# Performance work log

Measured on AMD Instinct MI355X. Metric: run time of the kernel, lower is better.

## Reference

```python
import jax, jax.numpy as jnp
import numpy as np

jax.config.update("jax_enable_x64", True)  # faithful int64 LIF state, as in the torch module

NUM_INPUTS = 700
NUM_HIDDEN = 4096
NUM_OUTPUT = 20
N_STEPS = 1000
ALPHA_SHIFT = 4   # synaptic-current decay shift
BETA_SHIFT = 3    # membrane decay shift
THRESHOLD = 1
BW1 = 64
BW2 = 64


def _sat(x, bw):
    # Quantize.saturate + to_int: clamp to signed bw-bit range, cast to int64.
    lo = -(2 ** (bw - 1))
    hi = 2 ** (bw - 1) - 1
    if jnp.issubdtype(x.dtype, jnp.floating):
        # values here are far below 2**63, so the float clip/cast is exact
        return jnp.clip(x, float(lo), float(hi)).astype(jnp.int64)
    return jnp.clip(x, lo, hi)


def _decay(v, shift):
    # LIF.exp_decay: v - (v >> shift) with arithmetic right shift on int64
    return v - (v >> shift)


def setup_inputs() -> dict:
    key = jax.random.key(0)
    k1, k2, k3, k4 = jax.random.split(key, 4)
    input_spikes = jax.random.randint(k1, (N_STEPS, NUM_INPUTS), 0, 2, dtype=jnp.int64)
    w1 = jax.random.randint(k2, (NUM_HIDDEN, NUM_INPUTS), -8, 8, dtype=jnp.int64)
    v1 = jax.random.randint(k3, (NUM_HIDDEN, NUM_HIDDEN), -8, 8, dtype=jnp.int64)
    w2 = jax.random.randint(k4, (NUM_OUTPUT, NUM_HIDDEN), -8, 8, dtype=jnp.int64)
    return {"input_spikes": input_spikes, "w1": w1, "v1": v1, "w2": w2}


def reference(input_spikes, w1, v1, w2):
    w1f = w1.astype(jnp.float32)
    v1f = v1.astype(jnp.float32)
    w2f = w2.astype(jnp.float32)
    # feed-forward input currents for all timesteps at once: [T, H]
    in_all = _sat(jnp.einsum("hi,ti->th", w1f, input_spikes.astype(jnp.float32)), BW1)

    H = w1.shape[0]
    O = w2.shape[0]
    z = lambda n: jnp.zeros((n,), dtype=jnp.int64)
    # state: hidden spikes, hidden mem, hidden syn, readout mem, readout syn
    init = (z(H), z(H), z(H), z(O), z(O))

    def step(state, in_cur):
        h_out, h_mem, h_syn, r_mem, r_syn = state
        # recurrent feedback current from PREVIOUS step's hidden spikes
        fb = _sat(jnp.einsum("hk,k->h", v1f, h_out.astype(jnp.float32)), BW1)
        syn_curr = _sat(in_cur + fb, BW1)
        # hidden LIF: reset (by previous spike) -> threshold -> decay/integrate
        h_mem = jnp.where(h_out == 1, 0, h_mem)
        new_out = (h_mem - THRESHOLD > 0).astype(jnp.int64)
        new_mem = _decay(h_mem, BETA_SHIFT) + h_syn
        new_syn = _decay(h_syn, ALPHA_SHIFT) + syn_curr
        # readout LIF (no reset); records updated membrane
        ro_cur = _sat(jnp.einsum("oh,h->o", w2f, new_out.astype(jnp.float32)), BW2)
        new_rmem = _decay(r_mem, BETA_SHIFT) + r_syn
        new_rsyn = _decay(r_syn, ALPHA_SHIFT) + ro_cur
        return (new_out, new_mem, new_syn, new_rmem, new_rsyn), new_rmem

    _, rec = jax.lax.scan(step, init, in_all)  # rec: [T, O]
    return rec.T  # torch.stack(ro_mem_rec, dim=1) -> [num_output, n_steps]
```

## Files before the change

### kernel.cpp

```cpp
#include <hip/hip_runtime.h>

#define T_STEPS 1000
#define N_IN    700
#define N_HID   4096
#define N_OUT   20
#define NBLK    64
#define HPB     64

typedef unsigned int u32x4 __attribute__((ext_vector_type(4)));

__device__ __forceinline__ u32x4 load_rec_sync(const u32x4* p) {
    u32x4 r;
    asm volatile("global_load_dwordx4 %0, %1, off sc0 sc1\n\t"
                 "s_waitcnt vmcnt(0)"
                 : "=v"(r) : "v"(p) : "memory");
    return r;
}
__device__ __forceinline__ void store_rec(u32x4* p, u32x4 v) {
    asm volatile("global_store_dwordx4 %0, %1, off sc0 sc1"
                 :: "v"(p), "v"(v) : "memory");
}

__global__ __launch_bounds__(256) void k_transpose_i8(
    const int* __restrict__ in, signed char* __restrict__ out,
    int R, int C, int out_stride)
{
    __shared__ signed char tile[32][33];
    const int cx = blockIdx.x * 32;
    const int ry = blockIdx.y * 32;
    const int tx = threadIdx.x;
    const int ty = threadIdx.y;
#pragma unroll
    for (int r = 0; r < 4; ++r) {
        int row = ry + ty + r * 8;
        int col = cx + tx;
        if (row < R && col < C)
            tile[ty + r * 8][tx] = (signed char)in[(size_t)row * C + col];
    }
    __syncthreads();
#pragma unroll
    for (int r = 0; r < 4; ++r) {
        int c   = cx + ty + r * 8;
        int row = ry + tx;
        if (c < C && row < R)
            out[(size_t)c * out_stride + row] = tile[tx][ty + r * 8];
    }
}

__global__ __launch_bounds__(256) void k_prep_v1(
    const int* __restrict__ in, unsigned char* __restrict__ out)
{
    __shared__ unsigned char tile[32][33];
    const int kx = blockIdx.x * 32;
    const int hy = blockIdx.y * 32;
    const int tx = threadIdx.x;
    const int ty = threadIdx.y;
#pragma unroll
    for (int r = 0; r < 4; ++r) {
        int h = hy + ty + r * 8;
        tile[ty + r * 8][tx] = (unsigned char)(in[(size_t)h * N_HID + kx + tx] + 8);
    }
    __syncthreads();
    const size_t bofs = (size_t)(hy >> 6) * (N_HID * 64) + (hy & 32);
#pragma unroll
    for (int r = 0; r < 4; ++r) {
        int k = kx + ty + r * 8;
        out[bofs + ((size_t)k << 6) + tx] = tile[tx][ty + r * 8];
    }
}

__global__ __launch_bounds__(256) void k_inall(
    const signed char* __restrict__ w1t,
    const int* __restrict__ spk,
    short* __restrict__ in_all2)
{
    __shared__ int s_spk[16][N_IN];
    const int t0 = blockIdx.y * 16;
    const int tcnt = min(16, T_STEPS - t0);
    const int tid = threadIdx.x;
    for (int b = 0; b < tcnt; ++b)
        for (int i = tid; i < N_IN; i += 256)
            s_spk[b][i] = spk[(size_t)(t0 + b) * N_IN + i];
    __syncthreads();
    const int h = blockIdx.x * 256 + tid;
    int acc[16];
#pragma unroll
    for (int b = 0; b < 16; ++b) acc[b] = 0;
    for (int i = 0; i < N_IN; ++i) {
        int w = (int)w1t[(size_t)i * N_HID + h];
#pragma unroll
        for (int b = 0; b < 16; ++b) acc[b] += w * s_spk[b][i];
    }
    const size_t base = (size_t)(h >> 6) * (T_STEPS * 64) + (h & 63);
    for (int b = 0; b < tcnt; ++b)
        in_all2[base + (size_t)(t0 + b) * 64] = (short)acc[b];
}

__global__ __launch_bounds__(256) void k_main(
    const short* __restrict__ in_all2,
    const unsigned char* __restrict__ v1b,
    u32x4* __restrict__ pub)
{
    const int tid  = threadIdx.x;
    const int wave = tid >> 6;
    const int lane = tid & 63;
    const int bid  = blockIdx.x;

    __shared__ u32x4 s_rec[2][NBLK];
    __shared__ unsigned int s_part[2][4][4][8];
    __shared__ int s_nw[2][4];

    int mm = 0, synv = 0, out_t = 0;

    const int mb = (wave << 4) | (lane >> 2);
    const unsigned char* gslot =
        v1b + ((size_t)bid << 18) + ((size_t)mb << 12) + ((lane & 3) << 4);
    const short* in_base = in_all2 + (size_t)bid * (T_STEPS * 64) + lane;

    if (tid == 0) { u32x4 v = {0u, 0u, 1u, 0u}; store_rec(pub + bid, v); }
    __syncthreads();

    for (int t = 0; t < T_STEPS; ++t) {
        const int cur = t & 1;
        int in_cur = 0;
        if (wave == 0) {
            int mem_t = (mm - (mm >> 3)) + synv;
            int mnext = out_t ? 0 : mem_t;
            int out_n = (mnext - 1 > 0) ? 1 : 0;
            unsigned long long om = __ballot(out_n);
            if (lane == 0) {
                u32x4 v = {(unsigned)om, (unsigned)(om >> 32), 1u, 0u};
                store_rec(pub + (size_t)(t + 1) * NBLK + bid, v);
            }
            in_cur = (int)in_base[t * 64];
            mm = mnext; out_t = out_n;
            __builtin_amdgcn_global_load_lds(
                (const void*)(pub + (size_t)t * NBLK + lane),
                (void*)&s_rec[cur ^ 1][0], 16, 0,  17);
        }

        unsigned int mlo = 0, mhi = 0;
        if (t > 0) {
            u32x4 rec = s_rec[cur][mb];
            if (rec.z == 0u) {
                const u32x4* rp = pub + (size_t)(t - 1) * NBLK + mb;
                do { __builtin_amdgcn_s_sleep(1); rec = load_rec_sync(rp); }
                while (rec.z == 0u);
            }
            mlo = rec.x; mhi = rec.y;
        }
        int myc = __popc(mlo) + __popc(mhi);

        unsigned int a0=0,a1=0,a2=0,a3=0,a4=0,a5=0,a6=0,a7=0;
        const unsigned int M = 0x00FF00FFu;
        {
            unsigned int m0 = mlo;
            while (m0) {
                int b = __builtin_ctz(m0); m0 &= m0 - 1;
                u32x4 v = *(const u32x4*)(gslot + ((size_t)b << 6));
                a0 += v.x & M;  a1 += (v.x >> 8) & M;
                a2 += v.y & M;  a3 += (v.y >> 8) & M;
                a4 += v.z & M;  a5 += (v.z >> 8) & M;
                a6 += v.w & M;  a7 += (v.w >> 8) & M;
            }
            unsigned int m1 = mhi;
            while (m1) {
                int b = __builtin_ctz(m1); m1 &= m1 - 1;
                u32x4 v = *(const u32x4*)(gslot + ((size_t)(b + 32) << 6));
                a0 += v.x & M;  a1 += (v.x >> 8) & M;
                a2 += v.y & M;  a3 += (v.y >> 8) & M;
                a4 += v.z & M;  a5 += (v.z >> 8) & M;
                a6 += v.w & M;  a7 += (v.w >> 8) & M;
            }
        }
#pragma unroll
        for (int s = 4; s <= 32; s <<= 1) {
            a0 += __shfl_xor(a0, s); a1 += __shfl_xor(a1, s);
            a2 += __shfl_xor(a2, s); a3 += __shfl_xor(a3, s);
            a4 += __shfl_xor(a4, s); a5 += __shfl_xor(a5, s);
            a6 += __shfl_xor(a6, s); a7 += __shfl_xor(a7, s);
            myc += __shfl_xor(myc, s);
        }
        if (lane == 0) s_nw[cur][wave] = myc;
        if (lane < 4) {
            unsigned int* sp = s_part[cur][wave][lane];
            sp[0]=a0; sp[1]=a1; sp[2]=a2; sp[3]=a3;
            sp[4]=a4; sp[5]=a5; sp[6]=a6; sp[7]=a7;
        }
        __syncthreads();

        if (wave == 0) {
            const int n = s_nw[cur][0] + s_nw[cur][1] + s_nw[cur][2] + s_nw[cur][3];
            const int li = lane >> 4, b = lane & 15;
            const int c = ((b >> 2) << 1) | (b & 1);
            const int half = (b >> 1) & 1;
            unsigned int s = s_part[cur][0][li][c] + s_part[cur][1][li][c]
                           + s_part[cur][2][li][c] + s_part[cur][3][li][c];
            int fb = (int)((s >> (half << 4)) & 0xFFFFu) - 8 * n;
            synv = (synv - (synv >> 4)) + in_cur + fb;
        }
    }
}

__global__ __launch_bounds__(256) void k_rocur(
    const int* __restrict__ w2,
    const u32x4* __restrict__ pub,
    int* __restrict__ ro)
{
    const int t = blockIdx.x;
    const int tid = threadIdx.x;
    __shared__ unsigned short s_list[N_HID];
    __shared__ int s_red[32][8];
    __shared__ int s_n;
    if (tid < 64) {
        u32x4 rec = pub[(size_t)t * NBLK + tid];
        unsigned long long m = (unsigned long long)rec.x |
                               ((unsigned long long)rec.y << 32);
        int cnt = __popcll(m);
        int inc = cnt;
#pragma unroll
        for (int d = 1; d < 64; d <<= 1) {
            int v = __shfl_up(inc, d);
            if (tid >= d) inc += v;
        }
        int p = inc - cnt;
        while (m) {
            s_list[p++] = (unsigned short)((tid << 6) | __builtin_ctzll(m));
            m &= m - 1;
        }
        if (tid == 63) s_n = inc;
    }
    __syncthreads();
    const int n = s_n;
    const int o = tid >> 3;
    const int r = tid & 7;
    if (o < N_OUT) {
        int acc = 0;
        for (int j = r; j < n; j += 8) acc += w2[(size_t)o * N_HID + s_list[j]];
        s_red[o][r] = acc;
    }
    __syncthreads();
    if (tid < N_OUT) {
        int acc = 0;
#pragma unroll
        for (int q = 0; q < 8; ++q) acc += s_red[tid][q];
        ro[(size_t)t * N_OUT + tid] = acc;
    }
}

#define CH 250
__global__ __launch_bounds__(256) void k_scan(const int* __restrict__ ro,
                                              int* __restrict__ out)
{
    __shared__ int s_ro[CH * N_OUT];
    __shared__ int s_out[CH * N_OUT];
    const int tid = threadIdx.x;
    int rm = 0, rs = 0;
    for (int c = 0; c < T_STEPS / CH; ++c) {
        for (int i = tid; i < CH * N_OUT; i += 256)
            s_ro[i] = ro[c * CH * N_OUT + i];
        __syncthreads();
        if (tid < N_OUT) {
            for (int j = 0; j < CH; ++j) {
                rm = (rm - (rm >> 3)) + rs;
                rs = (rs - (rs >> 4)) + s_ro[j * N_OUT + tid];
                s_out[j * N_OUT + tid] = rm;
            }
        }
        __syncthreads();
        for (int i = tid; i < CH * N_OUT; i += 256) {
            int o = i / CH, j = i - o * CH;
            out[o * T_STEPS + c * CH + j] = s_out[j * N_OUT + o];
        }
        __syncthreads();
    }
}

extern "C" void kernel_launch(void* const* d_in, const int* in_sizes, int n_in,
                              void* d_out, int out_size, void* d_ws, size_t ws_size,
                              hipStream_t stream)
{
    const int* spk = (const int*)d_in[0];
    const int* w1  = (const int*)d_in[1];
    const int* v1  = (const int*)d_in[2];
    const int* w2  = (const int*)d_in[3];
    int* out = (int*)d_out;

    char* ws = (char*)d_ws;
    constexpr size_t SZ_PUB    = (size_t)(T_STEPS + 1) * NBLK * 16;
    constexpr size_t OFF_PUB   = 0;
    constexpr size_t OFF_INALL = OFF_PUB + SZ_PUB;
    constexpr size_t OFF_V1B   = OFF_INALL + 8192000;
    constexpr size_t OFF_W1T   = OFF_V1B + 16777216;
    constexpr size_t OFF_RO    = OFF_W1T + 2867200;

    u32x4*          pub    = (u32x4*)(ws + OFF_PUB);
    short*          in_all = (short*)(ws + OFF_INALL);
    unsigned char*  v1b    = (unsigned char*)(ws + OFF_V1B);
    signed char*    w1t    = (signed char*)(ws + OFF_W1T);
    int*            ro     = (int*)(ws + OFF_RO);

    hipMemsetAsync(pub, 0, SZ_PUB, stream);

    dim3 tb(32, 8);
    k_prep_v1<<<dim3(128, 128), tb, 0, stream>>>(v1, v1b);
    k_transpose_i8<<<dim3(22, 128), tb, 0, stream>>>(w1, w1t, N_HID, N_IN, N_HID);
    k_inall<<<dim3(16, 63), 256, 0, stream>>>(w1t, spk, in_all);

    k_main<<<dim3(NBLK), dim3(256), 0, stream>>>(in_all, v1b, pub);

    k_rocur<<<dim3(T_STEPS), 256, 0, stream>>>(w2, pub, ro);
    k_scan<<<1, 256, 0, stream>>>(ro, out);
}
```

Measured before the change: 1.661 ms.

## Split recurrence across 256 single-wave blocks with nibble-packed weights in LDS

```diff
diff --git a/kernel.cpp b/kernel.cpp
--- a/kernel.cpp
+++ b/kernel.cpp
@@ -4,20 +4,21 @@
 #define N_IN    700
 #define N_HID   4096
 #define N_OUT   20
-#define NBLK    64
-#define HPB     64
+#define NBLK    256
+#define NPB     16
 
 typedef unsigned int u32x4 __attribute__((ext_vector_type(4)));
-
-__device__ __forceinline__ u32x4 load_rec_sync(const u32x4* p) {
-    u32x4 r;
-    asm volatile("global_load_dwordx4 %0, %1, off sc0 sc1\n\t"
+typedef unsigned int u32x2 __attribute__((ext_vector_type(2)));
+
+__device__ __forceinline__ unsigned load_rec4(const unsigned* p) {
+    unsigned r;
+    asm volatile("global_load_dword %0, %1, off sc0 sc1\n\t"
                  "s_waitcnt vmcnt(0)"
                  : "=v"(r) : "v"(p) : "memory");
     return r;
 }
-__device__ __forceinline__ void store_rec(u32x4* p, u32x4 v) {
-    asm volatile("global_store_dwordx4 %0, %1, off sc0 sc1"
+__device__ __forceinline__ void store_rec4(unsigned* p, unsigned v) {
+    asm volatile("global_store_dword %0, %1, off sc0 sc1"
                  :: "v"(p), "v"(v) : "memory");
 }
 
@@ -47,25 +48,28 @@
     }
 }
 
-__global__ __launch_bounds__(256) void k_prep_v1(
+__global__ __launch_bounds__(256) void k_prep_v1n(
     const int* __restrict__ in, unsigned char* __restrict__ out)
 {
-    __shared__ unsigned char tile[32][33];
-    const int kx = blockIdx.x * 32;
-    const int hy = blockIdx.y * 32;
-    const int tx = threadIdx.x;
-    const int ty = threadIdx.y;
+    __shared__ unsigned char tile[16][64];
+    const int k0 = blockIdx.x * 64;
+    const int b  = blockIdx.y;
+    const int t  = threadIdx.x;
+    const int kk = t & 63;
 #pragma unroll
     for (int r = 0; r < 4; ++r) {
-        int h = hy + ty + r * 8;
-        tile[ty + r * 8][tx] = (unsigned char)(in[(size_t)h * N_HID + kx + tx] + 8);
-    }
-    __syncthreads();
-    const size_t bofs = (size_t)(hy >> 6) * (N_HID * 64) + (hy & 32);
-#pragma unroll
-    for (int r = 0; r < 4; ++r) {
-        int k = kx + ty + r * 8;
-        out[bofs + ((size_t)k << 6) + tx] = tile[tx][ty + r * 8];
+        int hl = (t >> 6) + r * 4;
+        tile[hl][kk] = (unsigned char)(in[(size_t)(b * NPB + hl) * N_HID + k0 + kk] + 8);
+    }
+    __syncthreads();
+    if (t < 64) {
+        unsigned w0 = 0, w1 = 0;
+#pragma unroll
+        for (int j = 0; j < 8; ++j) w0 |= (unsigned)tile[j][t] << (4 * j);
+#pragma unroll
+        for (int j = 0; j < 8; ++j) w1 |= (unsigned)tile[8 + j][t] << (4 * j);
+        u32x2 v = {w0, w1};
+        *(u32x2*)(out + ((size_t)b << 15) + ((size_t)(k0 + t) << 3)) = v;
     }
 }
 
@@ -91,120 +95,117 @@
 #pragma unroll
         for (int b = 0; b < 16; ++b) acc[b] += w * s_spk[b][i];
     }
-    const size_t base = (size_t)(h >> 6) * (T_STEPS * 64) + (h & 63);
+    const size_t base = (size_t)(h >> 4) * (T_STEPS * NPB) + (h & 15);
     for (int b = 0; b < tcnt; ++b)
-        in_all2[base + (size_t)(t0 + b) * 64] = (short)acc[b];
-}
-
-__global__ __launch_bounds__(256) void k_main(
+        in_all2[base + (size_t)(t0 + b) * NPB] = (short)acc[b];
+}
+
+__global__ __launch_bounds__(64) void k_main(
     const short* __restrict__ in_all2,
-    const unsigned char* __restrict__ v1b,
-    u32x4* __restrict__ pub)
-{
-    const int tid  = threadIdx.x;
-    const int wave = tid >> 6;
-    const int lane = tid & 63;
+    const u32x2* __restrict__ v1n,
+    unsigned* __restrict__ pub)
+{
+    const int lane = threadIdx.x;
     const int bid  = blockIdx.x;
-
-    __shared__ u32x4 s_rec[2][NBLK];
-    __shared__ unsigned int s_part[2][4][4][8];
-    __shared__ int s_nw[2][4];
+    const int j    = lane & 15;
+
+    __shared__ u32x2 s_w[N_HID];
+    __shared__ u32x4 s_rec[2][64];
+
+    {
+        const u32x2* src = v1n + ((size_t)bid << 12);
+        for (int r = lane; r < N_HID; r += 64) s_w[r] = src[r];
+    }
+    asm volatile("s_waitcnt vmcnt(0) lgkmcnt(0)" ::: "memory");
+
+    if (lane == 0) store_rec4(pub + bid, 0x10000u);
 
     int mm = 0, synv = 0, out_t = 0;
-
-    const int mb = (wave << 4) | (lane >> 2);
-    const unsigned char* gslot =
-        v1b + ((size_t)bid << 18) + ((size_t)mb << 12) + ((lane & 3) << 4);
-    const short* in_base = in_all2 + (size_t)bid * (T_STEPS * 64) + lane;
-
-    if (tid == 0) { u32x4 v = {0u, 0u, 1u, 0u}; store_rec(pub + bid, v); }
-    __syncthreads();
+    const short* in_base = in_all2 + (size_t)bid * (T_STEPS * NPB) + j;
+    const u32x2* wl = s_w + (lane << 6);
+    const unsigned NM = 0x000F000Fu;
 
     for (int t = 0; t < T_STEPS; ++t) {
         const int cur = t & 1;
-        int in_cur = 0;
-        if (wave == 0) {
-            int mem_t = (mm - (mm >> 3)) + synv;
-            int mnext = out_t ? 0 : mem_t;
-            int out_n = (mnext - 1 > 0) ? 1 : 0;
-            unsigned long long om = __ballot(out_n);
-            if (lane == 0) {
-                u32x4 v = {(unsigned)om, (unsigned)(om >> 32), 1u, 0u};
-                store_rec(pub + (size_t)(t + 1) * NBLK + bid, v);
+        asm volatile("s_waitcnt vmcnt(0)" ::: "memory");
+        __builtin_amdgcn_sched_barrier(0);
+
+        int mem_t = (mm - (mm >> 3)) + synv;
+        int mnext = out_t ? 0 : mem_t;
+        int out_n = (mnext - 1 > 0) ? 1 : 0;
+        unsigned om = (unsigned)__ballot(out_n) & 0xFFFFu;
+        if (lane == 0) store_rec4(pub + (size_t)(t + 1) * NBLK + bid, 0x10000u | om);
+        mm = mnext; out_t = out_n;
+
+        int in_cur = (int)in_base[t * NPB];
+
+        __builtin_amdgcn_global_load_lds(
+            (const void*)(pub + (size_t)t * NBLK + (lane << 2)),
+            (void*)&s_rec[cur ^ 1][0], 16, 0,  17);
+
+        unsigned mlo = 0, mhi = 0;
+        if (t > 0) {
+            u32x4 q = s_rec[cur][lane];
+            if (((q.x & q.y & q.z & q.w) & 0x10000u) == 0u) {
+                const unsigned* rp = pub + (size_t)(t - 1) * NBLK + (lane << 2);
+                while (!(q.x & 0x10000u)) { __builtin_amdgcn_s_sleep(1); q.x = load_rec4(rp + 0); }
+                while (!(q.y & 0x10000u)) { __builtin_amdgcn_s_sleep(1); q.y = load_rec4(rp + 1); }
+                while (!(q.z & 0x10000u)) { __builtin_amdgcn_s_sleep(1); q.z = load_rec4(rp + 2); }
+                while (!(q.w & 0x10000u)) { __builtin_amdgcn_s_sleep(1); q.w = load_rec4(rp + 3); }
             }
-            in_cur = (int)in_base[t * 64];
-            mm = mnext; out_t = out_n;
-            __builtin_amdgcn_global_load_lds(
-                (const void*)(pub + (size_t)t * NBLK + lane),
-                (void*)&s_rec[cur ^ 1][0], 16, 0,  17);
-        }
-
-        unsigned int mlo = 0, mhi = 0;
-        if (t > 0) {
-            u32x4 rec = s_rec[cur][mb];
-            if (rec.z == 0u) {
-                const u32x4* rp = pub + (size_t)(t - 1) * NBLK + mb;
-                do { __builtin_amdgcn_s_sleep(1); rec = load_rec_sync(rp); }
-                while (rec.z == 0u);
-            }
-            mlo = rec.x; mhi = rec.y;
-        }
-        int myc = __popc(mlo) + __popc(mhi);
-
-        unsigned int a0=0,a1=0,a2=0,a3=0,a4=0,a5=0,a6=0,a7=0;
-        const unsigned int M = 0x00FF00FFu;
-        {
-            unsigned int m0 = mlo;
-            while (m0) {
-                int b = __builtin_ctz(m0); m0 &= m0 - 1;
-                u32x4 v = *(const u32x4*)(gslot + ((size_t)b << 6));
-                a0 += v.x & M;  a1 += (v.x >> 8) & M;
-                a2 += v.y & M;  a3 += (v.y >> 8) & M;
-                a4 += v.z & M;  a5 += (v.z >> 8) & M;
-                a6 += v.w & M;  a7 += (v.w >> 8) & M;
-            }
-            unsigned int m1 = mhi;
-            while (m1) {
-                int b = __builtin_ctz(m1); m1 &= m1 - 1;
-                u32x4 v = *(const u32x4*)(gslot + ((size_t)(b + 32) << 6));
-                a0 += v.x & M;  a1 += (v.x >> 8) & M;
-                a2 += v.y & M;  a3 += (v.y >> 8) & M;
-                a4 += v.z & M;  a5 += (v.z >> 8) & M;
-                a6 += v.w & M;  a7 += (v.w >> 8) & M;
-            }
-        }
-#pragma unroll
-        for (int s = 4; s <= 32; s <<= 1) {
+            mlo = (q.x & 0xFFFFu) | ((q.y & 0xFFFFu) << 16);
+            mhi = (q.z & 0xFFFFu) | ((q.w & 0xFFFFu) << 16);
+        }
+        unsigned long long m = ((unsigned long long)mhi << 32) | mlo;
+        int myc = __popcll(m);
+
+        unsigned a0=0,a1=0,a2=0,a3=0,a4=0,a5=0,a6=0,a7=0;
+#define ACC(v) do { \
+            a0 += (v).x & NM;         a1 += ((v).x >> 4)  & NM; \
+            a2 += ((v).x >> 8) & NM;  a3 += ((v).x >> 12) & NM; \
+            a4 += (v).y & NM;         a5 += ((v).y >> 4)  & NM; \
+            a6 += ((v).y >> 8) & NM;  a7 += ((v).y >> 12) & NM; } while (0)
+        u32x2 p0={0,0}, p1={0,0}, p2={0,0}, p3={0,0};
+        int b;
+        if (m) { b = __builtin_ctzll(m); m &= m - 1; p0 = wl[b]; }
+        if (m) { b = __builtin_ctzll(m); m &= m - 1; p1 = wl[b]; }
+        if (m) { b = __builtin_ctzll(m); m &= m - 1; p2 = wl[b]; }
+        if (m) { b = __builtin_ctzll(m); m &= m - 1; p3 = wl[b]; }
+        while (m) {
+            u32x2 n0={0,0}, n1={0,0}, n2={0,0}, n3={0,0};
+            if (m) { b = __builtin_ctzll(m); m &= m - 1; n0 = wl[b]; }
+            if (m) { b = __builtin_ctzll(m); m &= m - 1; n1 = wl[b]; }
+            if (m) { b = __builtin_ctzll(m); m &= m - 1; n2 = wl[b]; }
+            if (m) { b = __builtin_ctzll(m); m &= m - 1; n3 = wl[b]; }
+            ACC(p0); ACC(p1); ACC(p2); ACC(p3);
+            p0 = n0; p1 = n1; p2 = n2; p3 = n3;
+        }
+        ACC(p0); ACC(p1); ACC(p2); ACC(p3);
+#undef ACC
+
+#pragma unroll
+        for (int s = 1; s <= 32; s <<= 1) {
             a0 += __shfl_xor(a0, s); a1 += __shfl_xor(a1, s);
             a2 += __shfl_xor(a2, s); a3 += __shfl_xor(a3, s);
             a4 += __shfl_xor(a4, s); a5 += __shfl_xor(a5, s);
             a6 += __shfl_xor(a6, s); a7 += __shfl_xor(a7, s);
             myc += __shfl_xor(myc, s);
         }
-        if (lane == 0) s_nw[cur][wave] = myc;
-        if (lane < 4) {
-            unsigned int* sp = s_part[cur][wave][lane];
-            sp[0]=a0; sp[1]=a1; sp[2]=a2; sp[3]=a3;
-            sp[4]=a4; sp[5]=a5; sp[6]=a6; sp[7]=a7;
-        }
-        __syncthreads();
-
-        if (wave == 0) {
-            const int n = s_nw[cur][0] + s_nw[cur][1] + s_nw[cur][2] + s_nw[cur][3];
-            const int li = lane >> 4, b = lane & 15;
-            const int c = ((b >> 2) << 1) | (b & 1);
-            const int half = (b >> 1) & 1;
-            unsigned int s = s_part[cur][0][li][c] + s_part[cur][1][li][c]
-                           + s_part[cur][2][li][c] + s_part[cur][3][li][c];
-            int fb = (int)((s >> (half << 4)) & 0xFFFFu) - 8 * n;
-            synv = (synv - (synv >> 4)) + in_cur + fb;
-        }
+
+        unsigned g0 = (j & 1) ? a1 : a0, g1 = (j & 1) ? a3 : a2;
+        unsigned g2 = (j & 1) ? a5 : a4, g3 = (j & 1) ? a7 : a6;
+        unsigned h0 = (j & 2) ? g1 : g0, h1 = (j & 2) ? g3 : g2;
+        unsigned sel = (j & 8) ? h1 : h0;
+        int field = (j & 4) ? (int)(sel >> 16) : (int)(sel & 0xFFFFu);
+        int fb = field - 8 * myc;
+
+        synv = (synv - (synv >> 4)) + in_cur + fb;
     }
 }
 
 __global__ __launch_bounds__(256) void k_rocur(
     const int* __restrict__ w2,
-    const u32x4* __restrict__ pub,
+    const unsigned* __restrict__ pub,
     int* __restrict__ ro)
 {
     const int t = blockIdx.x;
@@ -213,9 +214,10 @@
     __shared__ int s_red[32][8];
     __shared__ int s_n;
     if (tid < 64) {
-        u32x4 rec = pub[(size_t)t * NBLK + tid];
-        unsigned long long m = (unsigned long long)rec.x |
-                               ((unsigned long long)rec.y << 32);
+        const unsigned* rp = pub + (size_t)t * NBLK + (tid << 2);
+        unsigned long long m =
+            (unsigned long long)((rp[0] & 0xFFFFu) | ((rp[1] & 0xFFFFu) << 16)) |
+            ((unsigned long long)((rp[2] & 0xFFFFu) | ((rp[3] & 0xFFFFu) << 16)) << 32);
         int cnt = __popcll(m);
         int inc = cnt;
 #pragma unroll
@@ -236,7 +238,7 @@
     const int r = tid & 7;
     if (o < N_OUT) {
         int acc = 0;
-        for (int j = r; j < n; j += 8) acc += w2[(size_t)o * N_HID + s_list[j]];
+        for (int jj = r; jj < n; jj += 8) acc += w2[(size_t)o * N_HID + s_list[jj]];
         s_red[o][r] = acc;
     }
     __syncthreads();
@@ -261,16 +263,16 @@
             s_ro[i] = ro[c * CH * N_OUT + i];
         __syncthreads();
         if (tid < N_OUT) {
-            for (int j = 0; j < CH; ++j) {
+            for (int jj = 0; jj < CH; ++jj) {
                 rm = (rm - (rm >> 3)) + rs;
-                rs = (rs - (rs >> 4)) + s_ro[j * N_OUT + tid];
-                s_out[j * N_OUT + tid] = rm;
+                rs = (rs - (rs >> 4)) + s_ro[jj * N_OUT + tid];
+                s_out[jj * N_OUT + tid] = rm;
             }
         }
         __syncthreads();
         for (int i = tid; i < CH * N_OUT; i += 256) {
-            int o = i / CH, j = i - o * CH;
-            out[o * T_STEPS + c * CH + j] = s_out[j * N_OUT + o];
+            int o = i / CH, jj = i - o * CH;
+            out[o * T_STEPS + c * CH + jj] = s_out[jj * N_OUT + o];
         }
         __syncthreads();
     }
@@ -287,27 +289,27 @@
     int* out = (int*)d_out;
 
     char* ws = (char*)d_ws;
-    constexpr size_t SZ_PUB    = (size_t)(T_STEPS + 1) * NBLK * 16;
+    constexpr size_t SZ_PUB    = (size_t)(T_STEPS + 1) * NBLK * 4;
     constexpr size_t OFF_PUB   = 0;
     constexpr size_t OFF_INALL = OFF_PUB + SZ_PUB;
-    constexpr size_t OFF_V1B   = OFF_INALL + 8192000;
-    constexpr size_t OFF_W1T   = OFF_V1B + 16777216;
+    constexpr size_t OFF_V1N   = OFF_INALL + 8192000;
+    constexpr size_t OFF_W1T   = OFF_V1N + 8388608;
     constexpr size_t OFF_RO    = OFF_W1T + 2867200;
 
-    u32x4*          pub    = (u32x4*)(ws + OFF_PUB);
+    unsigned*       pub    = (unsigned*)(ws + OFF_PUB);
     short*          in_all = (short*)(ws + OFF_INALL);
-    unsigned char*  v1b    = (unsigned char*)(ws + OFF_V1B);
+    unsigned char*  v1n    = (unsigned char*)(ws + OFF_V1N);
     signed char*    w1t    = (signed char*)(ws + OFF_W1T);
     int*            ro     = (int*)(ws + OFF_RO);
 
     hipMemsetAsync(pub, 0, SZ_PUB, stream);
 
     dim3 tb(32, 8);
-    k_prep_v1<<<dim3(128, 128), tb, 0, stream>>>(v1, v1b);
+    k_prep_v1n<<<dim3(64, 256), 256, 0, stream>>>(v1, v1n);
     k_transpose_i8<<<dim3(22, 128), tb, 0, stream>>>(w1, w1t, N_HID, N_IN, N_HID);
     k_inall<<<dim3(16, 63), 256, 0, stream>>>(w1t, spk, in_all);
 
-    k_main<<<dim3(NBLK), dim3(256), 0, stream>>>(in_all, v1b, pub);
+    k_main<<<dim3(NBLK), dim3(64), 0, stream>>>(in_all, (const u32x2*)v1n, pub);
 
     k_rocur<<<dim3(T_STEPS), 256, 0, stream>>>(w2, pub, ro);
     k_scan<<<1, 256, 0, stream>>>(ro, out);
```

After: 1.733 ms. +4.3%, slower.
